# Performance work log

Hardware: AMD Instinct MI355X
Metric: run time of the kernel (lower is better)

## Reference

```python
import jax, jax.numpy as jnp
import numpy as np
from jax import lax

N_SAMPLES = 2048
RADIUS = 0.2
K_GROUP = 32
BN_EPS = 1e-5


def furthest_point_sampling(xyz, n_samples):
    # xyz: [B, N, 3] -> indices [B, n_samples] (start from index 0)
    B, N, _ = xyz.shape

    def body(carry, _):
        dists, last = carry                                   # [B,N], [B]
        cur = jnp.take_along_axis(xyz, last[:, None, None], axis=1)  # [B,1,3]
        d = jnp.sum((xyz - cur) ** 2, axis=-1)                # [B,N]
        dists = jnp.minimum(dists, d)
        nxt = jnp.argmax(dists, axis=-1).astype(jnp.int32)    # [B]
        return (dists, nxt), nxt

    init = (jnp.full((B, N), 1e10, xyz.dtype), jnp.zeros((B,), jnp.int32))
    _, idxs = lax.scan(body, init, None, length=n_samples - 1)  # [n_samples-1, B]
    return jnp.concatenate([jnp.zeros((1, B), jnp.int32), idxs], axis=0).T  # [B,n_samples]


def ball_query(xyz, centroids, radius, k):
    # xyz: [B,N,3], centroids: [B,S,3] -> [B,S,k] neighbor indices within radius
    N = xyz.shape[1]
    d2 = jnp.sum((centroids[:, :, None, :] - xyz[:, None, :, :]) ** 2, axis=-1)  # [B,S,N]
    cand = jnp.where(d2 <= radius * radius, jnp.arange(N, dtype=jnp.int32), N)   # invalid -> N
    neg_topk, _ = lax.top_k(-cand, k)        # k smallest indices, ascending
    idx = -neg_topk                          # [B,S,k]
    first = idx[:, :, :1]                    # pad slots beyond valid count with first neighbor
    return jnp.where(idx == N, first, idx)


def batch_gather(data, idx):
    # data: [B,N,C], idx: [B,...] -> [B,...,C]
    return jax.vmap(lambda d, i: d[i])(data, idx)


def setup_inputs() -> dict:
    key = jax.random.key(0)
    ks = jax.random.split(key, 16)
    B, N, F = 8, 8192, 64
    inp = {
        "points_xyz": jax.random.uniform(ks[0], (B, N, 3), jnp.float32),
        "features": jax.random.normal(ks[1], (B, N, F), jnp.float32),
    }
    chans = [67, 64, 64, 128]
    for i in range(3):
        cin, cout = chans[i], chans[i + 1]
        scale = 1.0 / np.sqrt(cin)
        inp[f"w{i}"] = jax.random.uniform(ks[2 + 4 * i], (cout, cin), jnp.float32, -scale, scale)
        inp[f"b{i}"] = jax.random.uniform(ks[3 + 4 * i], (cout,), jnp.float32, -scale, scale)
        inp[f"g{i}"] = jnp.ones((cout,), jnp.float32)
        inp[f"beta{i}"] = jnp.zeros((cout,), jnp.float32)
    return inp


def reference(points_xyz, features, w0, b0, g0, beta0, w1, b1, g1, beta1, w2, b2, g2, beta2):
    B = points_xyz.shape[0]
    centroid_idx = furthest_point_sampling(points_xyz, N_SAMPLES)          # [B,S]
    centroids = jnp.take_along_axis(points_xyz, centroid_idx[:, :, None], axis=1)  # [B,S,3]
    grouped_idx = ball_query(points_xyz, centroids, RADIUS, K_GROUP)       # [B,S,K]
    grouped_xyz = batch_gather(points_xyz, grouped_idx)                    # [B,S,K,3]
    grouped_feat = batch_gather(features, grouped_idx)                     # [B,S,K,F]
    grouped_xyz_norm = grouped_xyz - centroids[:, :, None, :]
    x = jnp.concatenate([grouped_xyz_norm, grouped_feat], axis=-1)         # [B,S,K,C]

    for w, b, g, bt in ((w0, b0, g0, beta0), (w1, b1, g1, beta1), (w2, b2, g2, beta2)):
        x = jnp.einsum("bskc,oc->bsko", x, w) + b                          # 1x1 conv
        mean = jnp.mean(x, axis=(0, 1, 2))                                 # BN (train-mode batch stats)
        var = jnp.var(x, axis=(0, 1, 2))
        x = jax.nn.relu(g * (x - mean) * lax.rsqrt(var + BN_EPS) + bt)

    out = jnp.max(x, axis=2)                                               # max over group -> [B,S,Cout]
    return centroids, out
```

## Files before the change

### kernel.cpp

```cpp
#include <hip/hip_runtime.h>
#include <cstdint>
#include <cstddef>

#define NPTS 8192
#define NB 8
#define NS 2048
#define KG 32
#define NROWS (NB*NS*KG)
#define NREP 32

__device__ __forceinline__ float dist2_exact(float ax, float ay, float az,
                                             float bx, float by, float bz)
{
#pragma clang fp contract(off)
  float dx = ax - bx;
  float dy = ay - by;
  float dz = az - bz;
  return dx * dx + dy * dy + dz * dz;
}

__launch_bounds__(512)
__global__ void fps_kernel(const float* __restrict__ xyz, float* __restrict__ cents)
{
  __shared__ float sx[NPTS], sy[NPTS], sz[NPTS];
  __shared__ float scent[NS * 3];
  __shared__ unsigned long long spk[2][8];

  const int b = blockIdx.x;
  const int t = threadIdx.x;
  const float* base = xyz + (size_t)b * NPTS * 3;

  float px[16], py[16], pz[16], dmin[16];
  unsigned lo[16];
#pragma unroll
  for (int j = 0; j < 16; ++j) {
    int i = j * 512 + t;
    float x = base[3*i+0], y = base[3*i+1], z = base[3*i+2];
    px[j] = x; py[j] = y; pz[j] = z;
    dmin[j] = 1e10f;
    lo[j] = ~(unsigned)i;
    sx[i] = x; sy[i] = y; sz[i] = z;
  }

  float cx = base[0], cy = base[1], cz = base[2];
  if (t == 0) { scent[0] = cx; scent[1] = cy; scent[2] = cz; }
  __syncthreads();

  for (int it = 1; it < NS; ++it) {
    unsigned long long best = 0ull;
#pragma unroll
    for (int j = 0; j < 16; ++j) {
      float d = dist2_exact(px[j], py[j], pz[j], cx, cy, cz);
      float m = fminf(dmin[j], d);
      dmin[j] = m;
      unsigned long long p = ((unsigned long long)__float_as_uint(m) << 32)
                           | (unsigned long long)lo[j];
      best = (p > best) ? p : best;
    }
#pragma unroll
    for (int off = 32; off > 0; off >>= 1) {
      unsigned long long op = __shfl_xor(best, off, 64);
      best = (op > best) ? op : best;
    }
    const int pb = it & 1;
    if ((t & 63) == 0) spk[pb][t >> 6] = best;
    __syncthreads();
    unsigned long long bb = spk[pb][0];
#pragma unroll
    for (int q = 1; q < 8; ++q) {
      unsigned long long oq = spk[pb][q];
      bb = (oq > bb) ? oq : bb;
    }
    const int win = (int)(~(unsigned)bb);
    cx = sx[win]; cy = sy[win]; cz = sz[win];
    if (t == 0) { scent[3*it] = cx; scent[3*it+1] = cy; scent[3*it+2] = cz; }
  }
  __syncthreads();
  float* cb = cents + (size_t)b * NS * 3;
  for (int q = t; q < NS * 3; q += 512) cb[q] = scent[q];
}

__launch_bounds__(256)
__global__ void ballq_kernel(const float* __restrict__ xyz,
                             const float* __restrict__ cents,
                             int* __restrict__ gidx)
{
  const int gid  = blockIdx.x * 256 + threadIdx.x;
  const int w    = gid >> 6;
  const int lane = gid & 63;
  const int b    = w >> 11;
  const float* base = xyz + (size_t)b * NPTS * 3;
  const float cx = cents[3*w+0], cy = cents[3*w+1], cz = cents[3*w+2];
  const float R2 = (float)(0.2 * 0.2);
  int* out = gidx + (size_t)w * KG;

  int filled = 0, first = -1;
  for (int c = 0; c < NPTS/64; ++c) {
    int i = (c << 6) | lane;
    float d = dist2_exact(base[3*i+0], base[3*i+1], base[3*i+2], cx, cy, cz);
    bool inb = (d <= R2);
    unsigned long long mask = __ballot(inb);
    if (first < 0 && mask) first = (c << 6) + (__ffsll((long long)mask) - 1);
    int pre  = __popcll(mask & ((1ull << lane) - 1ull));
    int slot = filled + pre;
    if (inb && slot < KG) out[slot] = i;
    filled += __popcll(mask);
    if (filled >= KG) break;
  }
  if (filled < KG && lane < KG && lane >= filled) out[lane] = first;
}

template<int H>
__device__ __forceinline__ void fold_sum_step(float* a, int lane) {
#pragma unroll
  for (int q = 0; q < H; ++q) {
    float keep = (lane & H) ? a[q + H] : a[q];
    float send = (lane & H) ? a[q] : a[q + H];
    a[q] = keep + __shfl_xor(send, H, 64);
  }
}

__device__ __forceinline__ float fold_sum16(float* a, int lane) {
  fold_sum_step<8>(a, lane);
  fold_sum_step<4>(a, lane);
  fold_sum_step<2>(a, lane);
  fold_sum_step<1>(a, lane);
  float v = a[0];
  v += __shfl_xor(v, 16, 64);
  v += __shfl_xor(v, 32, 64);
  return v;
}

template<int H>
__device__ __forceinline__ void fold_max_step(float* a, int lane) {
#pragma unroll
  for (int q = 0; q < H; ++q) {
    float keep = (lane & H) ? a[q + H] : a[q];
    float send = (lane & H) ? a[q] : a[q + H];
    a[q] = fmaxf(keep, __shfl_xor(send, H, 64));
  }
}

__device__ __forceinline__ float fold_max16(float* a, int lane) {
  fold_max_step<8>(a, lane);
  fold_max_step<4>(a, lane);
  fold_max_step<2>(a, lane);
  fold_max_step<1>(a, lane);
  float v = a[0];
  v = fmaxf(v, __shfl_xor(v, 16, 64));
  return v;
}

template<int H>
__device__ __forceinline__ void fold_min_step(float* a, int lane) {
#pragma unroll
  for (int q = 0; q < H; ++q) {
    float keep = (lane & H) ? a[q + H] : a[q];
    float send = (lane & H) ? a[q] : a[q + H];
    a[q] = fminf(keep, __shfl_xor(send, H, 64));
  }
}

__device__ __forceinline__ float fold_min16(float* a, int lane) {
  fold_min_step<8>(a, lane);
  fold_min_step<4>(a, lane);
  fold_min_step<2>(a, lane);
  fold_min_step<1>(a, lane);
  float v = a[0];
  v = fminf(v, __shfl_xor(v, 16, 64));
  return v;
}

__device__ __forceinline__ void stats16(float* y, int lane, int o0,
                                        float* __restrict__ gs1,
                                        float* __restrict__ gs2)
{
  float sq[16];
#pragma unroll
  for (int q = 0; q < 16; ++q) sq[q] = y[q] * y[q];
  float s1 = fold_sum16(y, lane);
  float s2 = fold_sum16(sq, lane);
  if (lane < 16)       atomicAdd(&gs1[o0 + lane], s1);
  else if (lane < 32)  atomicAdd(&gs2[o0 + (lane & 15)], s2);
}

__device__ __forceinline__ void minmax16(const float* y, int lane, int o0, int cs,
                                         float* __restrict__ zmax,
                                         float* __restrict__ zmin)
{
  float ymx[16], ymn[16];
#pragma unroll
  for (int q = 0; q < 16; ++q) { ymx[q] = y[q]; ymn[q] = y[q]; }
  float mx = fold_max16(ymx, lane);
  float mn = fold_min16(ymn, lane);
  if (!(lane & 16)) {
    zmax[(size_t)cs * 128 + o0 + (lane & 15)] = mx;
    zmin[(size_t)cs * 128 + o0 + (lane & 15)] = mn;
  }
}

__device__ __forceinline__ unsigned short f2b(float f) {
  unsigned b = __float_as_uint(f);
  return (unsigned short)((b + 0x7FFFu + ((b >> 16) & 1u)) >> 16);
}
__device__ __forceinline__ float b2f(unsigned short h) {
  return __uint_as_float(((unsigned)h) << 16);
}

__launch_bounds__(256, 3)
__global__ void k1_kernel(const float* __restrict__ xyz, const float* __restrict__ feats,
                          const float* __restrict__ cents, const int* __restrict__ gidx,
                          const float* __restrict__ w0, const float* __restrict__ b0,
                          float* __restrict__ stats, unsigned short* __restrict__ actL)
{
  const int t = threadIdx.x, lane = t & 63;
  const int r = blockIdx.x * 256 + t;
  const int b = r >> 16, cs = r >> 5;
  const int i = gidx[r];
  const int rep = (blockIdx.x * 4 + (t >> 6)) & (NREP - 1);
  const float* pp = xyz + ((size_t)(b << 13) + i) * 3;
  const float* cc = cents + (size_t)cs * 3;
  const float* fb = feats + (((size_t)(b << 13) + i) << 6);

  float xin[67];
  xin[0] = pp[0] - cc[0]; xin[1] = pp[1] - cc[1]; xin[2] = pp[2] - cc[2];
  const float4* f4 = (const float4*)fb;
#pragma unroll
  for (int q = 0; q < 16; ++q) {
    float4 v = f4[q];
    xin[3+4*q+0] = v.x; xin[3+4*q+1] = v.y; xin[3+4*q+2] = v.z; xin[3+4*q+3] = v.w;
  }

  for (int o0 = 0; o0 < 64; o0 += 16) {
    float y[16];
#pragma unroll
    for (int k = 0; k < 16; ++k) {
      float a = b0[o0 + k];
#pragma unroll
      for (int c = 0; c < 67; ++c)
        a = fmaf(w0[(o0 + k)*67 + c], xin[c], a);
      y[k] = a;
    }
#pragma unroll
    for (int k = 0; k < 16; ++k)
      actL[(size_t)(o0 + k) * NROWS + r] = f2b(y[k]);
    stats16(y, lane, o0, stats + (size_t)rep*64, stats + 2048 + (size_t)rep*64);
  }
}

__launch_bounds__(256, 3)
__global__ void k2_kernel(unsigned short* __restrict__ actL,
                          const float* __restrict__ w1, const float* __restrict__ b1,
                          const float* __restrict__ prm,
                          float* __restrict__ stats)
{
  const int t = threadIdx.x, lane = t & 63;
  const int r = blockIdx.x * 256 + t;
  const int rep = (blockIdx.x * 4 + (t >> 6)) & (NREP - 1);

  float x[64];
#pragma unroll
  for (int c = 0; c < 64; ++c)
    x[c] = b2f(actL[(size_t)c * NROWS + r]);
#pragma unroll
  for (int c = 0; c < 64; ++c)
    x[c] = fmaxf(fmaf(prm[c], x[c], prm[64 + c]), 0.f);

  for (int o0 = 0; o0 < 64; o0 += 16) {
    float y[16];
#pragma unroll
    for (int k = 0; k < 16; ++k) {
      float a = b1[o0 + k];
#pragma unroll
      for (int c = 0; c < 64; ++c)
        a = fmaf(w1[(o0 + k)*64 + c], x[c], a);
      y[k] = a;
    }
#pragma unroll
    for (int k = 0; k < 16; ++k)
      actL[(size_t)(o0 + k) * NROWS + r] = f2b(y[k]);
    stats16(y, lane, o0, stats + 4096 + (size_t)rep*64, stats + 6144 + (size_t)rep*64);
  }
}

__launch_bounds__(256, 3)
__global__ void k3_kernel(const unsigned short* __restrict__ actL,
                          const float* __restrict__ w2, const float* __restrict__ b2,
                          const float* __restrict__ prm,
                          float* __restrict__ stats,
                          float* __restrict__ zmax, float* __restrict__ zmin)
{
  const int t = threadIdx.x, lane = t & 63;
  const int r = blockIdx.x * 256 + t;
  const int cs = r >> 5;
  const int rep = (blockIdx.x * 4 + (t >> 6)) & (NREP - 1);

  float x[64];
#pragma unroll
  for (int c = 0; c < 64; ++c)
    x[c] = b2f(actL[(size_t)c * NROWS + r]);
#pragma unroll
  for (int c = 0; c < 64; ++c)
    x[c] = fmaxf(fmaf(prm[128 + c], x[c], prm[192 + c]), 0.f);

  for (int o0 = 0; o0 < 128; o0 += 16) {
    float y[16];
#pragma unroll
    for (int k = 0; k < 16; ++k) {
      float a = b2[o0 + k];
#pragma unroll
      for (int c = 0; c < 64; ++c)
        a = fmaf(w2[(o0 + k)*64 + c], x[c], a);
      y[k] = a;
    }
    minmax16(y, lane, o0, cs, zmax, zmin);
    stats16(y, lane, o0, stats + 8192 + (size_t)rep*128, stats + 12288 + (size_t)rep*128);
  }
}

__launch_bounds__(256)
__global__ void outfin_kernel(const float* __restrict__ zmax,
                              const float* __restrict__ zmin,
                              const float* __restrict__ prm,
                              float* __restrict__ outp)
{
  int i = blockIdx.x * 256 + threadIdx.x;
  int ch = i & 127;
  float a = prm[256 + ch], sh = prm[384 + ch];
  float z = (a >= 0.f) ? zmax[i] : zmin[i];
  outp[i] = fmaxf(fmaf(a, z, sh), 0.f);
}

template<int MODE>
__launch_bounds__(256, (MODE <= 2 ? 4 : 2))
__global__ void chain_kernel(const float* __restrict__ xyz,
                             const float* __restrict__ feats,
                             const float* __restrict__ cents,
                             const int* __restrict__ gidx,
                             const float* __restrict__ w0, const float* __restrict__ b0,
                             const float* __restrict__ w1, const float* __restrict__ b1,
                             const float* __restrict__ w2, const float* __restrict__ b2,
                             const float* __restrict__ prm,
                             float* __restrict__ stats,
                             float* __restrict__ outp,
                             float* __restrict__ zmax, float* __restrict__ zmin)
{
  const int t    = threadIdx.x;
  const int lane = t & 63;
  const int r    = blockIdx.x * 256 + t;
  const int b    = r >> 16;
  const int cs   = r >> 5;
  const int i    = gidx[r];
  const int rep  = (blockIdx.x * 4 + (t >> 6)) & (NREP - 1);

  const float* pp = xyz + ((size_t)(b << 13) + i) * 3;
  const float* cc = cents + (size_t)cs * 3;
  const float* fb = feats + (((size_t)(b << 13) + i) << 6);

  float acc[64];
  {
    float c0 = pp[0] - cc[0], c1 = pp[1] - cc[1], c2 = pp[2] - cc[2];
#pragma unroll
    for (int o = 0; o < 64; ++o)
      acc[o] = fmaf(w0[o*67+2], c2, fmaf(w0[o*67+1], c1, fmaf(w0[o*67+0], c0, b0[o])));
  }
  for (int c0 = 0; c0 < 64; c0 += 16) {
    float xc[16];
    const float4* f4 = (const float4*)(fb + c0);
    float4 v0 = f4[0], v1 = f4[1], v2 = f4[2], v3 = f4[3];
    xc[0]=v0.x; xc[1]=v0.y; xc[2]=v0.z; xc[3]=v0.w;
    xc[4]=v1.x; xc[5]=v1.y; xc[6]=v1.z; xc[7]=v1.w;
    xc[8]=v2.x; xc[9]=v2.y; xc[10]=v2.z; xc[11]=v2.w;
    xc[12]=v3.x; xc[13]=v3.y; xc[14]=v3.z; xc[15]=v3.w;
#pragma unroll
    for (int o = 0; o < 64; ++o) {
      float a = acc[o];
#pragma unroll
      for (int ci = 0; ci < 16; ++ci)
        a = fmaf(w0[o*67 + 3 + c0 + ci], xc[ci], a);
      acc[o] = a;
    }
  }

  if (MODE == 1) {
#pragma unroll
    for (int o0 = 0; o0 < 64; o0 += 16) {
      float y[16];
#pragma unroll
      for (int q = 0; q < 16; ++q) y[q] = acc[o0 + q];
      stats16(y, lane, o0, stats + (size_t)rep*64, stats + 2048 + (size_t)rep*64);
    }
    return;
  }

#pragma unroll
  for (int o = 0; o < 64; ++o)
    acc[o] = fmaxf(fmaf(prm[o], acc[o], prm[64 + o]), 0.f);

  if (MODE == 2) {
    for (int o0 = 0; o0 < 64; o0 += 16) {
      float y[16];
#pragma unroll
      for (int k = 0; k < 16; ++k) {
        float a = b1[o0 + k];
#pragma unroll
        for (int c = 0; c < 64; ++c)
          a = fmaf(w1[(o0 + k)*64 + c], acc[c], a);
        y[k] = a;
      }
      stats16(y, lane, o0, stats + 4096 + (size_t)rep*64, stats + 6144 + (size_t)rep*64);
    }
    return;
  }

  float y1[64];
#pragma unroll
  for (int o = 0; o < 64; ++o) {
    float a = b1[o];
#pragma unroll
    for (int c = 0; c < 64; ++c)
      a = fmaf(w1[o*64 + c], acc[c], a);
    y1[o] = a;
  }
#pragma unroll
  for (int o = 0; o < 64; ++o)
    y1[o] = fmaxf(fmaf(prm[128 + o], y1[o], prm[192 + o]), 0.f);

  if (MODE == 3 || MODE == 5) {
    for (int o0 = 0; o0 < 128; o0 += 16) {
      float y[16];
#pragma unroll
      for (int k = 0; k < 16; ++k) {
        float a = b2[o0 + k];
#pragma unroll
        for (int c = 0; c < 64; ++c)
          a = fmaf(w2[(o0 + k)*64 + c], y1[c], a);
        y[k] = a;
      }
      if (MODE == 5) minmax16(y, lane, o0, cs, zmax, zmin);
      stats16(y, lane, o0, stats + 8192 + (size_t)rep*128, stats + 12288 + (size_t)rep*128);
    }
    return;
  }

  for (int o0 = 0; o0 < 128; o0 += 16) {
    float y[16];
#pragma unroll
    for (int k = 0; k < 16; ++k) {
      float a = b2[o0 + k];
#pragma unroll
      for (int c = 0; c < 64; ++c)
        a = fmaf(w2[(o0 + k)*64 + c], y1[c], a);
      y[k] = a;
    }
#pragma unroll
    for (int k = 0; k < 16; ++k)
      y[k] = fmaxf(fmaf(prm[256 + o0 + k], y[k], prm[384 + o0 + k]), 0.f);
    float m = fold_max16(y, lane);
    if (!(lane & 16))
      outp[(size_t)cs * 128 + o0 + (lane & 15)] = m;
  }
}

__global__ void finalize_kernel(const float* __restrict__ stats,
                                const float* __restrict__ g,
                                const float* __restrict__ beta,
                                float* __restrict__ pa, float* __restrict__ psh, int C)
{
  int c = threadIdx.x;
  if (c >= C) return;
  float s1 = 0.f, s2 = 0.f;
  for (int rr = 0; rr < NREP; ++rr) { s1 += stats[rr*C + c]; s2 += stats[NREP*C + rr*C + c]; }
  const float invn = 1.0f / (float)NROWS;
  float mean = s1 * invn;
  float var  = s2 * invn - mean * mean;
  float rs   = 1.0f / sqrtf(var + 1e-5f);
  float a    = g[c] * rs;
  pa[c]  = a;
  psh[c] = fmaf(-mean, a, beta[c]);
}

__global__ void zero_kernel(float* __restrict__ p, int n)
{
  int i = blockIdx.x * 256 + threadIdx.x;
  if (i < n) p[i] = 0.f;
}

extern "C" void kernel_launch(void* const* d_in, const int* in_sizes, int n_in,
                              void* d_out, int out_size, void* d_ws, size_t ws_size,
                              hipStream_t stream)
{
  (void)in_sizes; (void)n_in; (void)out_size;
  const float* xyz   = (const float*)d_in[0];
  const float* feats = (const float*)d_in[1];
  const float* w0 = (const float*)d_in[2],  *b0 = (const float*)d_in[3];
  const float* g0 = (const float*)d_in[4],  *bt0 = (const float*)d_in[5];
  const float* w1 = (const float*)d_in[6],  *b1 = (const float*)d_in[7];
  const float* g1 = (const float*)d_in[8],  *bt1 = (const float*)d_in[9];
  const float* w2 = (const float*)d_in[10], *b2 = (const float*)d_in[11];
  const float* g2 = (const float*)d_in[12], *bt2 = (const float*)d_in[13];

  float* cents = (float*)d_out;
  float* outp  = cents + (size_t)NB * NS * 3;

  char* wsb = (char*)d_ws;
  int*   gidx  = (int*)wsb;
  float* stats = (float*)(wsb + (2ull << 20));
  float* prm   = stats + 16384;
  float* zmax  = (float*)(wsb + (4ull  << 20));
  float* zmin  = (float*)(wsb + (12ull << 20));
  unsigned short* actL = (unsigned short*)(wsb + (20ull << 20));
  const size_t need_A = (20ull << 20) + (size_t)NROWS * 64 * 2;
  const size_t need_B = (20ull << 20);

  zero_kernel<<<64, 256, 0, stream>>>(stats, 16384);
  fps_kernel<<<NB, 512, 0, stream>>>(xyz, cents);
  ballq_kernel<<<(NB*NS*64)/256, 256, 0, stream>>>(xyz, cents, gidx);

  if (ws_size >= need_A) {
    k1_kernel<<<NROWS/256, 256, 0, stream>>>(xyz, feats, cents, gidx, w0, b0, stats, actL);
    finalize_kernel<<<1, 128, 0, stream>>>(stats + 0, g0, bt0, prm + 0, prm + 64, 64);
    k2_kernel<<<NROWS/256, 256, 0, stream>>>(actL, w1, b1, prm, stats);
    finalize_kernel<<<1, 128, 0, stream>>>(stats + 4096, g1, bt1, prm + 128, prm + 192, 64);
    k3_kernel<<<NROWS/256, 256, 0, stream>>>(actL, w2, b2, prm, stats, zmax, zmin);
    finalize_kernel<<<1, 128, 0, stream>>>(stats + 8192, g2, bt2, prm + 256, prm + 384, 128);
    outfin_kernel<<<(16384*128)/256, 256, 0, stream>>>(zmax, zmin, prm, outp);
  } else if (ws_size >= need_B) {
    chain_kernel<1><<<NROWS/256, 256, 0, stream>>>(xyz, feats, cents, gidx,
        w0, b0, w1, b1, w2, b2, prm, stats, outp, zmax, zmin);
    finalize_kernel<<<1, 128, 0, stream>>>(stats + 0, g0, bt0, prm + 0, prm + 64, 64);
    chain_kernel<2><<<NROWS/256, 256, 0, stream>>>(xyz, feats, cents, gidx,
        w0, b0, w1, b1, w2, b2, prm, stats, outp, zmax, zmin);
    finalize_kernel<<<1, 128, 0, stream>>>(stats + 4096, g1, bt1, prm + 128, prm + 192, 64);
    chain_kernel<5><<<NROWS/256, 256, 0, stream>>>(xyz, feats, cents, gidx,
        w0, b0, w1, b1, w2, b2, prm, stats, outp, zmax, zmin);
    finalize_kernel<<<1, 128, 0, stream>>>(stats + 8192, g2, bt2, prm + 256, prm + 384, 128);
    outfin_kernel<<<(16384*128)/256, 256, 0, stream>>>(zmax, zmin, prm, outp);
  } else {
    chain_kernel<1><<<NROWS/256, 256, 0, stream>>>(xyz, feats, cents, gidx,
        w0, b0, w1, b1, w2, b2, prm, stats, outp, zmax, zmin);
    finalize_kernel<<<1, 128, 0, stream>>>(stats + 0, g0, bt0, prm + 0, prm + 64, 64);
    chain_kernel<2><<<NROWS/256, 256, 0, stream>>>(xyz, feats, cents, gidx,
        w0, b0, w1, b1, w2, b2, prm, stats, outp, zmax, zmin);
    finalize_kernel<<<1, 128, 0, stream>>>(stats + 4096, g1, bt1, prm + 128, prm + 192, 64);
    chain_kernel<3><<<NROWS/256, 256, 0, stream>>>(xyz, feats, cents, gidx,
        w0, b0, w1, b1, w2, b2, prm, stats, outp, zmax, zmin);
    finalize_kernel<<<1, 128, 0, stream>>>(stats + 8192, g2, bt2, prm + 256, prm + 384, 128);
    chain_kernel<4><<<NROWS/256, 256, 0, stream>>>(xyz, feats, cents, gidx,
        w0, b0, w1, b1, w2, b2, prm, stats, outp, zmax, zmin);
  }
}
```

Measured before the change: 2.860 ms.

## Morton-sort points and prune FPS wavefront updates with bounding boxes

Adds a per-batch counting sort that reorders points by 3D Morton cell, so each FPS wavefront owns a spatially compact chunk of 1024 points. Each wavefront computes its chunk's bounding box. On each iteration it skips the distance update when the box is farther from the new centroid than the wave's current maximum min-distance, since none of its min-distances could change. The original index is packed into the tie-break key so argmax ties still resolve to the smallest original index. The cost is an extra sort kernel, extra workspace buffers, and a small safety margin on the box test that must stay exact against float rounding.

Result: faster. 2.535 ms (-11.3%).

```diff
diff --git a/kernel.cpp b/kernel.cpp
--- a/kernel.cpp
+++ b/kernel.cpp
@@ -19,8 +19,51 @@
   return dx * dx + dy * dy + dz * dz;
 }
 
+__device__ __forceinline__ unsigned mort3(unsigned v) {
+  return (v & 1u) | ((v & 2u) << 2) | ((v & 4u) << 4);
+}
+
+__launch_bounds__(256)
+__global__ void sort_kernel(const float* __restrict__ xyz,
+                            float* __restrict__ sX, float* __restrict__ sY,
+                            float* __restrict__ sZ, unsigned* __restrict__ sO)
+{
+  __shared__ unsigned hist[512];
+  __shared__ unsigned startv[512];
+  __shared__ unsigned short cellid[NPTS];
+  const int b = blockIdx.x, t = threadIdx.x;
+  const float* base = xyz + (size_t)b * NPTS * 3;
+
+  for (int q = t; q < 512; q += 256) hist[q] = 0u;
+  __syncthreads();
+  for (int q = t; q < NPTS; q += 256) {
+    float x = base[3*q], y = base[3*q+1], z = base[3*q+2];
+    int ix = (int)(x * 8.f); ix = ix < 0 ? 0 : (ix > 7 ? 7 : ix);
+    int iy = (int)(y * 8.f); iy = iy < 0 ? 0 : (iy > 7 ? 7 : iy);
+    int iz = (int)(z * 8.f); iz = iz < 0 ? 0 : (iz > 7 ? 7 : iz);
+    unsigned m = mort3((unsigned)ix) | (mort3((unsigned)iy) << 1) | (mort3((unsigned)iz) << 2);
+    cellid[q] = (unsigned short)m;
+    atomicAdd(&hist[m], 1u);
+  }
+  __syncthreads();
+  if (t == 0) {
+    unsigned run = 0;
+    for (int i = 0; i < 512; ++i) { unsigned h = hist[i]; startv[i] = run; run += h; }
+  }
+  __syncthreads();
+  for (int q = t; q < NPTS; q += 256) {
+    unsigned m = cellid[q];
+    unsigned pos = atomicAdd(&startv[m], 1u);
+    size_t o = (size_t)b * NPTS + pos;
+    sX[o] = base[3*q]; sY[o] = base[3*q+1]; sZ[o] = base[3*q+2];
+    sO[o] = (unsigned)q;
+  }
+}
+
 __launch_bounds__(512)
-__global__ void fps_kernel(const float* __restrict__ xyz, float* __restrict__ cents)
+__global__ void fps_kernel(const float* __restrict__ sX, const float* __restrict__ sY,
+                           const float* __restrict__ sZ, const unsigned* __restrict__ sO,
+                           const float* __restrict__ xyz, float* __restrict__ cents)
 {
   __shared__ float sx[NPTS], sy[NPTS], sz[NPTS];
   __shared__ float scent[NS * 3];
@@ -28,42 +71,70 @@
 
   const int b = blockIdx.x;
   const int t = threadIdx.x;
-  const float* base = xyz + (size_t)b * NPTS * 3;
+  const int w = t >> 6, lane = t & 63;
+  const size_t sb = (size_t)b * NPTS;
 
   float px[16], py[16], pz[16], dmin[16];
   unsigned lo[16];
 #pragma unroll
   for (int j = 0; j < 16; ++j) {
-    int i = j * 512 + t;
-    float x = base[3*i+0], y = base[3*i+1], z = base[3*i+2];
+    int i = w * 1024 + j * 64 + lane;
+    float x = sX[sb + i], y = sY[sb + i], z = sZ[sb + i];
     px[j] = x; py[j] = y; pz[j] = z;
     dmin[j] = 1e10f;
-    lo[j] = ~(unsigned)i;
+    lo[j] = ~((sO[sb + i] << 13) | (unsigned)i);
     sx[i] = x; sy[i] = y; sz[i] = z;
   }
-
-  float cx = base[0], cy = base[1], cz = base[2];
+  float bxl = px[0], bxh = px[0], byl = py[0], byh = py[0], bzl = pz[0], bzh = pz[0];
+#pragma unroll
+  for (int j = 1; j < 16; ++j) {
+    bxl = fminf(bxl, px[j]); bxh = fmaxf(bxh, px[j]);
+    byl = fminf(byl, py[j]); byh = fmaxf(byh, py[j]);
+    bzl = fminf(bzl, pz[j]); bzh = fmaxf(bzh, pz[j]);
+  }
+#pragma unroll
+  for (int off = 1; off <= 32; off <<= 1) {
+    bxl = fminf(bxl, __shfl_xor(bxl, off, 64)); bxh = fmaxf(bxh, __shfl_xor(bxh, off, 64));
+    byl = fminf(byl, __shfl_xor(byl, off, 64)); byh = fmaxf(byh, __shfl_xor(byh, off, 64));
+    bzl = fminf(bzl, __shfl_xor(bzl, off, 64)); bzh = fmaxf(bzh, __shfl_xor(bzh, off, 64));
+  }
+
+  unsigned long long bestc = ((unsigned long long)__float_as_uint(1e10f) << 32);
+
+  const float* o0 = xyz + sb * 3;
+  float cx = o0[0], cy = o0[1], cz = o0[2];
   if (t == 0) { scent[0] = cx; scent[1] = cy; scent[2] = cz; }
   __syncthreads();
 
   for (int it = 1; it < NS; ++it) {
-    unsigned long long best = 0ull;
-#pragma unroll
-    for (int j = 0; j < 16; ++j) {
-      float d = dist2_exact(px[j], py[j], pz[j], cx, cy, cz);
-      float m = fminf(dmin[j], d);
-      dmin[j] = m;
-      unsigned long long p = ((unsigned long long)__float_as_uint(m) << 32)
-                           | (unsigned long long)lo[j];
-      best = (p > best) ? p : best;
-    }
-#pragma unroll
-    for (int off = 32; off > 0; off >>= 1) {
-      unsigned long long op = __shfl_xor(best, off, 64);
-      best = (op > best) ? op : best;
+    float qx = cx - fminf(fmaxf(cx, bxl), bxh);
+    float qy = cy - fminf(fmaxf(cy, byl), byh);
+    float qz = cz - fminf(fmaxf(cz, bzl), bzh);
+    float dbox2 = (qx*qx + qy*qy + qz*qz) * 0.999f;
+    float tmaxw = __uint_as_float((unsigned)(bestc >> 32));
+    if (dbox2 < tmaxw) {
+      float bm = -1.0f;
+      unsigned lb = 0u;
+#pragma unroll
+      for (int j = 0; j < 16; ++j) {
+        float d = dist2_exact(px[j], py[j], pz[j], cx, cy, cz);
+        float m = fminf(dmin[j], d);
+        dmin[j] = m;
+        bool take = (m > bm);
+        bm = take ? m : bm;
+        lb = take ? lo[j] : lb;
+      }
+      unsigned long long best = ((unsigned long long)__float_as_uint(bm) << 32)
+                              | (unsigned long long)lb;
+#pragma unroll
+      for (int off = 32; off > 0; off >>= 1) {
+        unsigned long long op = __shfl_xor(best, off, 64);
+        best = (op > best) ? op : best;
+      }
+      bestc = best;
     }
     const int pb = it & 1;
-    if ((t & 63) == 0) spk[pb][t >> 6] = best;
+    if (lane == 0) spk[pb][w] = bestc;
     __syncthreads();
     unsigned long long bb = spk[pb][0];
 #pragma unroll
@@ -71,7 +142,7 @@
       unsigned long long oq = spk[pb][q];
       bb = (oq > bb) ? oq : bb;
     }
-    const int win = (int)(~(unsigned)bb);
+    const int win = (int)((~(unsigned)bb) & 8191u);
     cx = sx[win]; cy = sy[win]; cz = sz[win];
     if (t == 0) { scent[3*it] = cx; scent[3*it+1] = cy; scent[3*it+2] = cz; }
   }
@@ -507,6 +578,10 @@
   int*   gidx  = (int*)wsb;
   float* stats = (float*)(wsb + (2ull << 20));
   float* prm   = stats + 16384;
+  float* sX = (float*)(wsb + (2ull << 20) + (512u << 10));
+  float* sY = sX + (size_t)NB * NPTS;
+  float* sZ = sY + (size_t)NB * NPTS;
+  unsigned* sO = (unsigned*)(sZ + (size_t)NB * NPTS);
   float* zmax  = (float*)(wsb + (4ull  << 20));
   float* zmin  = (float*)(wsb + (12ull << 20));
   unsigned short* actL = (unsigned short*)(wsb + (20ull << 20));
@@ -514,7 +589,8 @@
   const size_t need_B = (20ull << 20);
 
   zero_kernel<<<64, 256, 0, stream>>>(stats, 16384);
-  fps_kernel<<<NB, 512, 0, stream>>>(xyz, cents);
+  sort_kernel<<<NB, 256, 0, stream>>>(xyz, sX, sY, sZ, sO);
+  fps_kernel<<<NB, 512, 0, stream>>>(sX, sY, sZ, sO, xyz, cents);
   ballq_kernel<<<(NB*NS*64)/256, 256, 0, stream>>>(xyz, cents, gidx);
 
   if (ws_size >= need_A) {
```
